# Kernel tuning notes

Measured on AMD Instinct MI355X. Metric: run time of the kernel, lower is better.

## Reference

```python
import jax, jax.numpy as jnp
import numpy as np

WS = 7        # window size
NH = 6        # num heads

def window_partition(x, ws):
    # x: (B, H, W, C) -> (B*nW, ws*ws, C)
    B, H, W, C = x.shape
    x = x.reshape(B, H // ws, ws, W // ws, ws, C)
    x = x.transpose(0, 1, 3, 2, 4, 5)
    return x.reshape(-1, ws * ws, C)

def setup_inputs() -> dict:
    key = jax.random.key(0)
    k1, k2, k3 = jax.random.split(key, 3)
    B, C, H, W = 8, 192, 224, 224
    x = jax.random.normal(k1, (B, C, H, W), dtype=jnp.float32)
    W_qk = jax.random.normal(k2, (2 * C, C), dtype=jnp.float32) * 0.02
    b_qk = jax.random.normal(k3, (2 * C,), dtype=jnp.float32) * 0.02
    return {"x": x, "W_qk": W_qk, "b_qk": b_qk}

def reference(x, W_qk, b_qk):
    B, C, H, W = x.shape
    hd = C // NH
    scale = hd ** (-0.5)
    xw = window_partition(x.transpose(0, 2, 3, 1), WS)      # (BnW, 49, C)
    qk = xw @ W_qk.T + b_qk                                  # (BnW, 49, 2C)
    qk = qk.reshape(-1, WS * WS, 2, NH, hd)
    q = qk[:, :, 0] * scale                                  # (BnW, 49, NH, hd)
    k = qk[:, :, 1]
    attn = jnp.einsum('bnhd,bmhd->bhnm', q, k)               # (BnW, NH, 49, 49)
    return jax.nn.softmax(attn, axis=-1)
```

## Files before the change

### kernel.cpp

```cpp
#include <hip/hip_runtime.h>
#include <hip/hip_bf16.h>
#include <math.h>
#include <stdint.h>

#define CCH   192
#define HWD   224
#define NWIN  8192
#define NPIX  49
#define KDIM  192
#define NHEAD 6
#define ROWB  (KDIM * 2)
#define MULQ  0.2550348616845977f

typedef __bf16 bf16x8 __attribute__((ext_vector_type(8)));
typedef __bf16 bf16x2 __attribute__((ext_vector_type(2)));
typedef float  f32x4  __attribute__((ext_vector_type(4)));

__global__ void wconv_kernel(const float* __restrict__ w,
                             const float* __restrict__ bq,
                             uint16_t* __restrict__ wbf) {
    int o = blockIdx.x * 256 + threadIdx.x;
    if (o >= 384 * 192) return;
    if (o < 384) {
        float bb = bq[o];
        if (o < 192) bb *= MULQ;
        ((float*)(wbf + 384 * 192))[o] = bb;
    }
    int e  = o & 7;
    int t  = o >> 3;
    int lr = t & 15;  t >>= 4;
    int lg = t & 3;   t >>= 2;
    int kk = t % 6;
    int ng = t / 6;
    int col  = ng * 16 + lr;
    int kcol = kk * 32 + lg * 8 + e;
    float wv = w[col * KDIM + kcol];
    if (col < 192) wv *= MULQ;
    __bf16 v = (__bf16)wv;
    wbf[o] = __builtin_bit_cast(uint16_t, v);
}

__global__ __launch_bounds__(1024, 8)
void attn_win_kernel(const float* __restrict__ x,
                     const uint16_t* __restrict__ wbf,
                     float* __restrict__ out) {
    __shared__ uint16_t ldsA[NPIX * KDIM];
    __shared__ uint16_t ldsB[NPIX * KDIM];

    const int tid  = threadIdx.x;
    const int wave = tid >> 6;
    const int l    = tid & 63;
    const int lg   = l >> 4;
    const int lr   = l & 15;

    const int win = ((blockIdx.x & 7) << 10) | (blockIdx.x >> 3);
    const int b   = win >> 10;
    const int wh  = (win >> 5) & 31;
    const int ww  = win & 31;
    const int h0 = wh * 7, w0 = ww * 7;

    const float* bias = (const float*)(wbf + 384 * 192);

    if (l < NPIX) {
        int r = (l * 37) >> 8;
        int s = l - r * 7;
        const float* xp = x + (size_t)(b * CCH + wave * 12) * (HWD * HWD)
                            + (h0 + r) * HWD + (w0 + s);
        float g[12];
        #pragma unroll
        for (int c = 0; c < 12; ++c)
            g[c] = xp[(size_t)c * (HWD * HWD)];
        const uint32_t rb  = (uint32_t)(l * ROWB + wave * 24);
        const uint32_t swz = (uint32_t)((l & 7) << 4);
        #pragma unroll
        for (int c = 0; c < 12; c += 2) {
            bf16x2 p = { (__bf16)g[c], (__bf16)g[c + 1] };
            uint32_t byte = (rb + (uint32_t)(c * 2)) ^ swz;
            *(uint32_t*)((char*)ldsA + byte) = __builtin_bit_cast(uint32_t, p);
        }
    }
    __syncthreads();

    const int mp = wave & 1;
    const int cg = wave >> 1;
    f32x4 acc[2][3];
    #pragma unroll
    for (int nt = 0; nt < 3; ++nt) {
        float bb = bias[cg * 48 + nt * 16 + lr];
        #pragma unroll
        for (int mt = 0; mt < 2; ++mt)
            acc[mt][nt] = f32x4{bb, bb, bb, bb};
    }

    #pragma unroll
    for (int kk = 0; kk < 6; ++kk) {
        bf16x8 afr[2];
        #pragma unroll
        for (int mt = 0; mt < 2; ++mt) {
            int row = mp * 32 + mt * 16 + lr;
            if (row > 48) row = 48;
            int byte = (row * ROWB + kk * 64 + lg * 16) ^ ((row & 7) << 4);
            afr[mt] = *(const bf16x8*)((const char*)ldsA + byte);
        }
        bf16x8 bfr[3];
        #pragma unroll
        for (int nt = 0; nt < 3; ++nt)
            bfr[nt] = *(const bf16x8*)(
                wbf + (((cg * 3 + nt) * 6 + kk) * 4 + lg) * 128 + lr * 8);
        #pragma unroll
        for (int nt = 0; nt < 3; ++nt)
            #pragma unroll
            for (int mt = 0; mt < 2; ++mt)
                acc[mt][nt] = __builtin_amdgcn_mfma_f32_16x16x32_bf16(
                    afr[mt], bfr[nt], acc[mt][nt], 0, 0, 0);
    }
    __syncthreads();

    {
        const bool isq = (cg < 4);
        uint16_t* dst = isq ? ldsA : ldsB;
        #pragma unroll
        for (int nt = 0; nt < 3; ++nt) {
            int colW = cg * 48 + nt * 16 + lr;
            int jj = isq ? colW : (colW - 192);
            #pragma unroll
            for (int mt = 0; mt < 2; ++mt) {
                #pragma unroll
                for (int r = 0; r < 4; ++r) {
                    int row = mp * 32 + mt * 16 + lg * 4 + r;
                    if (row < NPIX) {
                        __bf16 bv = (__bf16)acc[mt][nt][r];
                        *(__bf16*)((char*)dst +
                            ((row * ROWB + jj * 2) ^ ((row & 7) << 4))) = bv;
                    }
                }
            }
        }
    }
    __syncthreads();

    float* outw = out + (size_t)win * (NHEAD * NPIX * NPIX);
    const int qt    = wave & 3;
    const int qrow  = qt * 16 + lr;
    const int qrc   = qrow > 48 ? 48 : qrow;
    const uint32_t qswz = (uint32_t)((qrc & 7) << 4);

    auto do_head = [&](int h) {
        const bf16x8 qfr = *(const bf16x8*)((const char*)ldsA +
            (((uint32_t)(qrc * ROWB + h * 64 + lg * 16)) ^ qswz));

        float v[16];
        #pragma unroll
        for (int nt2 = 0; nt2 < 4; ++nt2) {
            int krow = nt2 * 16 + lr;
            if (krow > 48) krow = 48;
            const bf16x8 kfr = *(const bf16x8*)((const char*)ldsB +
                (((uint32_t)(krow * ROWB + h * 64 + lg * 16)) ^ ((krow & 7) << 4)));
            f32x4 p = __builtin_amdgcn_mfma_f32_16x16x32_bf16(
                kfr, qfr, f32x4{0.f, 0.f, 0.f, 0.f}, 0, 0, 0);
            #pragma unroll
            for (int r = 0; r < 4; ++r) {
                int k = nt2 * 16 + lg * 4 + r;
                v[nt2 * 4 + r] = (k < NPIX) ? p[r] : -INFINITY;
            }
        }

        float m = v[0];
        #pragma unroll
        for (int i = 1; i < 16; ++i) m = fmaxf(m, v[i]);
        m = fmaxf(m, __shfl_xor(m, 16, 64));
        m = fmaxf(m, __shfl_xor(m, 32, 64));

        float sum = 0.f;
        #pragma unroll
        for (int i = 0; i < 16; ++i) {
            v[i] = exp2f(v[i] - m);
            sum += v[i];
        }
        sum += __shfl_xor(sum, 16, 64);
        sum += __shfl_xor(sum, 32, 64);
        const float inv = __fdividef(1.0f, sum);

        if (qrow < NPIX) {
            float* orow = outw + h * (NPIX * NPIX) + qrow * NPIX;
            #pragma unroll
            for (int nt2 = 0; nt2 < 3; ++nt2)
                #pragma unroll
                for (int r = 0; r < 4; ++r)
                    orow[nt2 * 16 + lg * 4 + r] = v[nt2 * 4 + r] * inv;
            if (lg == 0) orow[48] = v[12] * inv;
        }
    };

    const int h1 = wave >> 2;
    do_head(h1);
    if (wave < 8) do_head(h1 + 4);
}

extern "C" void kernel_launch(void* const* d_in, const int* in_sizes, int n_in,
                              void* d_out, int out_size, void* d_ws, size_t ws_size,
                              hipStream_t stream) {
    const float* x  = (const float*)d_in[0];
    const float* W  = (const float*)d_in[1];
    const float* bq = (const float*)d_in[2];
    float* out = (float*)d_out;
    uint16_t* wbf = (uint16_t*)d_ws;

    wconv_kernel<<<(384 * 192 + 255) / 256, 256, 0, stream>>>(W, bq, wbf);
    attn_win_kernel<<<NWIN, 1024, 0, stream>>>(x, wbf, out);
}
```

Baseline: 313.5 us.

## Process two adjacent windows per block with separate LDS buffers

Each block now handles two horizontally adjacent windows. It loads both windows' inputs up front and keeps separate Q/K LDS buffers so that window 1's GEMM can overlap window 0's softmax without an intervening barrier. The head assignment for the second window is rebalanced so different waves take the extra head, and bias loads are hoisted and shared across both windows. The cost is six window-sized LDS buffers per block (about 113 KB of dynamic shared memory) and fewer resident blocks, which may reduce latency hiding.

```diff
diff --git a/kernel.cpp b/kernel.cpp
--- a/kernel.cpp
+++ b/kernel.cpp
@@ -10,6 +10,15 @@
 #define KDIM  192
 #define NHEAD 6
 #define ROWB  (KDIM * 2)
+#define NBLK  (NWIN / 2)
+#define WSZ   (NPIX * KDIM * 2)
+#define X0O   0
+#define X1O   (1 * WSZ)
+#define Q0O   (2 * WSZ)
+#define K0O   (3 * WSZ)
+#define Q1O   (4 * WSZ)
+#define K1O   (5 * WSZ)
+#define LDSSZ (6 * WSZ)
 #define MULQ  0.2550348616845977f
 
 typedef __bf16 bf16x8 __attribute__((ext_vector_type(8)));
@@ -40,12 +49,11 @@
     wbf[o] = __builtin_bit_cast(uint16_t, v);
 }
 
-__global__ __launch_bounds__(1024, 8)
-void attn_win_kernel(const float* __restrict__ x,
-                     const uint16_t* __restrict__ wbf,
-                     float* __restrict__ out) {
-    __shared__ uint16_t ldsA[NPIX * KDIM];
-    __shared__ uint16_t ldsB[NPIX * KDIM];
+__global__ __launch_bounds__(1024, 4)
+void attn_win2_kernel(const float* __restrict__ x,
+                      const uint16_t* __restrict__ wbf,
+                      float* __restrict__ out) {
+    extern __shared__ char smem[];
 
     const int tid  = threadIdx.x;
     const int wave = tid >> 6;
@@ -53,72 +61,80 @@
     const int lg   = l >> 4;
     const int lr   = l & 15;
 
-    const int win = ((blockIdx.x & 7) << 10) | (blockIdx.x >> 3);
-    const int b   = win >> 10;
-    const int wh  = (win >> 5) & 31;
-    const int ww  = win & 31;
-    const int h0 = wh * 7, w0 = ww * 7;
-
-    const float* bias = (const float*)(wbf + 384 * 192);
+    const int blk  = (int)blockIdx.x;
+    const int blk2 = (blk & 7) * (NBLK / 8) + (blk >> 3);
+    const int wbase = blk2 * 2;
+    const int b    = wbase >> 10;
+    const int wh   = (wbase >> 5) & 31;
+    const int ww0  = wbase & 31;
+    const int h0   = wh * 7, w0p = ww0 * 7;
+
+    const float* biasp = (const float*)(wbf + 384 * 192);
+    const int mp = wave & 1;
+    const int cg = wave >> 1;
+    float bias0[3];
+    #pragma unroll
+    for (int nt = 0; nt < 3; ++nt)
+        bias0[nt] = biasp[cg * 48 + nt * 16 + lr];
+
+    const size_t HW2 = (size_t)HWD * HWD;
 
     if (l < NPIX) {
         int r = (l * 37) >> 8;
         int s = l - r * 7;
-        const float* xp = x + (size_t)(b * CCH + wave * 12) * (HWD * HWD)
-                            + (h0 + r) * HWD + (w0 + s);
-        float g[12];
-        #pragma unroll
-        for (int c = 0; c < 12; ++c)
-            g[c] = xp[(size_t)c * (HWD * HWD)];
+        const float* xp = x + (size_t)(b * CCH + wave * 12) * HW2
+                            + (size_t)(h0 + r) * HWD + (w0p + s);
+        float g0[12], g1[12];
+        #pragma unroll
+        for (int c = 0; c < 12; ++c) g0[c] = xp[(size_t)c * HW2];
+        #pragma unroll
+        for (int c = 0; c < 12; ++c) g1[c] = xp[(size_t)c * HW2 + 7];
         const uint32_t rb  = (uint32_t)(l * ROWB + wave * 24);
         const uint32_t swz = (uint32_t)((l & 7) << 4);
         #pragma unroll
         for (int c = 0; c < 12; c += 2) {
-            bf16x2 p = { (__bf16)g[c], (__bf16)g[c + 1] };
+            bf16x2 p0 = { (__bf16)g0[c], (__bf16)g0[c + 1] };
+            bf16x2 p1 = { (__bf16)g1[c], (__bf16)g1[c + 1] };
             uint32_t byte = (rb + (uint32_t)(c * 2)) ^ swz;
-            *(uint32_t*)((char*)ldsA + byte) = __builtin_bit_cast(uint32_t, p);
+            *(uint32_t*)(smem + X0O + byte) = __builtin_bit_cast(uint32_t, p0);
+            *(uint32_t*)(smem + X1O + byte) = __builtin_bit_cast(uint32_t, p1);
         }
     }
     __syncthreads();
 
-    const int mp = wave & 1;
-    const int cg = wave >> 1;
-    f32x4 acc[2][3];
-    #pragma unroll
-    for (int nt = 0; nt < 3; ++nt) {
-        float bb = bias[cg * 48 + nt * 16 + lr];
-        #pragma unroll
-        for (int mt = 0; mt < 2; ++mt)
-            acc[mt][nt] = f32x4{bb, bb, bb, bb};
-    }
-
-    #pragma unroll
-    for (int kk = 0; kk < 6; ++kk) {
-        bf16x8 afr[2];
-        #pragma unroll
-        for (int mt = 0; mt < 2; ++mt) {
-            int row = mp * 32 + mt * 16 + lr;
-            if (row > 48) row = 48;
-            int byte = (row * ROWB + kk * 64 + lg * 16) ^ ((row & 7) << 4);
-            afr[mt] = *(const bf16x8*)((const char*)ldsA + byte);
-        }
-        bf16x8 bfr[3];
-        #pragma unroll
-        for (int nt = 0; nt < 3; ++nt)
-            bfr[nt] = *(const bf16x8*)(
-                wbf + (((cg * 3 + nt) * 6 + kk) * 4 + lg) * 128 + lr * 8);
-        #pragma unroll
-        for (int nt = 0; nt < 3; ++nt)
+    auto gemm1_stage = [&](const char* xb, char* qb, char* kb) {
+        f32x4 acc[2][3];
+        #pragma unroll
+        for (int nt = 0; nt < 3; ++nt) {
+            float bb = bias0[nt];
             #pragma unroll
             for (int mt = 0; mt < 2; ++mt)
-                acc[mt][nt] = __builtin_amdgcn_mfma_f32_16x16x32_bf16(
-                    afr[mt], bfr[nt], acc[mt][nt], 0, 0, 0);
-    }
-    __syncthreads();
-
-    {
+                acc[mt][nt] = f32x4{bb, bb, bb, bb};
+        }
+        #pragma unroll
+        for (int kk = 0; kk < 6; ++kk) {
+            bf16x8 afr[2];
+            #pragma unroll
+            for (int mt = 0; mt < 2; ++mt) {
+                int row = mp * 32 + mt * 16 + lr;
+                if (row > 48) row = 48;
+                int byte = (row * ROWB + kk * 64 + lg * 16) ^ ((row & 7) << 4);
+                afr[mt] = *(const bf16x8*)(xb + byte);
+            }
+            bf16x8 bfr[3];
+            #pragma unroll
+            for (int nt = 0; nt < 3; ++nt)
+                bfr[nt] = *(const bf16x8*)(
+                    wbf + (((cg * 3 + nt) * 6 + kk) * 4 + lg) * 128 + lr * 8);
+            #pragma unroll
+            for (int nt = 0; nt < 3; ++nt)
+                #pragma unroll
+                for (int mt = 0; mt < 2; ++mt)
+                    acc[mt][nt] = __builtin_amdgcn_mfma_f32_16x16x32_bf16(
+                        afr[mt], bfr[nt], acc[mt][nt], 0, 0, 0);
+        }
         const bool isq = (cg < 4);
-        uint16_t* dst = isq ? ldsA : ldsB;
+        char* dst = isq ? qb : kb;
         #pragma unroll
         for (int nt = 0; nt < 3; ++nt) {
             int colW = cg * 48 + nt * 16 + lr;
@@ -130,23 +146,22 @@
                     int row = mp * 32 + mt * 16 + lg * 4 + r;
                     if (row < NPIX) {
                         __bf16 bv = (__bf16)acc[mt][nt][r];
-                        *(__bf16*)((char*)dst +
+                        *(__bf16*)(dst +
                             ((row * ROWB + jj * 2) ^ ((row & 7) << 4))) = bv;
                     }
                 }
             }
         }
-    }
-    __syncthreads();
-
-    float* outw = out + (size_t)win * (NHEAD * NPIX * NPIX);
+    };
+
     const int qt    = wave & 3;
     const int qrow  = qt * 16 + lr;
     const int qrc   = qrow > 48 ? 48 : qrow;
     const uint32_t qswz = (uint32_t)((qrc & 7) << 4);
-
-    auto do_head = [&](int h) {
-        const bf16x8 qfr = *(const bf16x8*)((const char*)ldsA +
+    const int h1 = wave >> 2;
+
+    auto do_head = [&](int h, const char* qb, const char* kb, float* outw) {
+        const bf16x8 qfr = *(const bf16x8*)(qb +
             (((uint32_t)(qrc * ROWB + h * 64 + lg * 16)) ^ qswz));
 
         float v[16];
@@ -154,7 +169,7 @@
         for (int nt2 = 0; nt2 < 4; ++nt2) {
             int krow = nt2 * 16 + lr;
             if (krow > 48) krow = 48;
-            const bf16x8 kfr = *(const bf16x8*)((const char*)ldsB +
+            const bf16x8 kfr = *(const bf16x8*)(kb +
                 (((uint32_t)(krow * ROWB + h * 64 + lg * 16)) ^ ((krow & 7) << 4)));
             f32x4 p = __builtin_amdgcn_mfma_f32_16x16x32_bf16(
                 kfr, qfr, f32x4{0.f, 0.f, 0.f, 0.f}, 0, 0, 0);
@@ -192,9 +207,18 @@
         }
     };
 
-    const int h1 = wave >> 2;
-    do_head(h1);
-    if (wave < 8) do_head(h1 + 4);
+    float* outw0 = out + (size_t)wbase * (NHEAD * NPIX * NPIX);
+    float* outw1 = outw0 + (NHEAD * NPIX * NPIX);
+
+    gemm1_stage(smem + X0O, smem + Q0O, smem + K0O);
+    __syncthreads();
+    do_head(h1, smem + Q0O, smem + K0O, outw0);
+    if (wave < 8) do_head(h1 + 4, smem + Q0O, smem + K0O, outw0);
+
+    gemm1_stage(smem + X1O, smem + Q1O, smem + K1O);
+    __syncthreads();
+    do_head(h1, smem + Q1O, smem + K1O, outw1);
+    if (wave >= 8) do_head(h1 + 2, smem + Q1O, smem + K1O, outw1);
 }
 
 extern "C" void kernel_launch(void* const* d_in, const int* in_sizes, int n_in,
@@ -207,5 +231,5 @@
     uint16_t* wbf = (uint16_t*)d_ws;
 
     wconv_kernel<<<(384 * 192 + 255) / 256, 256, 0, stream>>>(W, bq, wbf);
-    attn_win_kernel<<<NWIN, 1024, 0, stream>>>(x, wbf, out);
+    attn_win2_kernel<<<NBLK, 1024, LDSSZ, stream>>>(x, wbf, out);
 }
```

After: 321.4 us. +2.5%, slower.
